# Optimization experiments

Measured on AMD Instinct MI355X. Metric: run time of the kernel, lower is better.

## Reference

```python
import jax, jax.numpy as jnp
import numpy as np

NMIX = 10  # mixtures in discretized mix of logistics


def _causal_mask(kh, kw, include_center):
    # rows strictly above center fully visible; center row left of center; optionally center
    m = np.zeros((kh, kw), dtype=np.float32)
    m[: kh // 2, :] = 1.0
    m[kh // 2, : kw // 2] = 1.0
    if include_center:
        m[kh // 2, kw // 2] = 1.0
    return jnp.asarray(m)[None, None]  # [1,1,kh,kw] broadcast over O,I


def _conv(x, w):
    return jax.lax.conv_general_dilated(
        x, w, (1, 1), 'SAME', dimension_numbers=('NCHW', 'OIHW', 'NCHW'))


def pixelcnn_params(x, w_in, w_blk, w_out1, w_out2):
    mA = _causal_mask(7, 7, False)
    mB = _causal_mask(3, 3, True)
    h = _conv(x, w_in * mA)                      # [B,160,H,W]
    for i in range(w_blk.shape[0]):              # 5 gated resnet blocks
        g = _conv(jax.nn.relu(h), w_blk[i] * mB)  # [B,320,H,W]
        a, b = jnp.split(g, 2, axis=1)
        h = h + jnp.tanh(a) * jax.nn.sigmoid(b)
    h = jax.nn.relu(_conv(jax.nn.relu(h), w_out1))
    return _conv(h, w_out2)                      # [B,100,H,W]


def dmol_log_prob(x, params):
    # x: [B,3,H,W] in [-1,1]; params: [B,100,H,W]; returns per-example log prob [B]
    B, C, H, W = x.shape
    l = jnp.transpose(params, (0, 2, 3, 1))       # [B,H,W,100]
    xt = jnp.transpose(x, (0, 2, 3, 1))           # [B,H,W,3]
    logit_probs = l[..., :NMIX]                   # [B,H,W,10]
    rest = l[..., NMIX:].reshape(B, H, W, 3, 3 * NMIX)
    means = rest[..., :NMIX]
    log_scales = jnp.maximum(rest[..., NMIX:2 * NMIX], -7.0)
    coeffs = jnp.tanh(rest[..., 2 * NMIX:])
    xe = xt[..., None]                            # [B,H,W,3,1]
    m1 = means[..., 0, :]
    m2 = means[..., 1, :] + coeffs[..., 0, :] * xe[..., 0, :]
    m3 = means[..., 2, :] + coeffs[..., 1, :] * xe[..., 0, :] + coeffs[..., 2, :] * xe[..., 1, :]
    means_adj = jnp.stack([m1, m2, m3], axis=3)   # [B,H,W,3,10]
    centered = xe - means_adj
    inv_stdv = jnp.exp(-log_scales)
    plus_in = inv_stdv * (centered + 1.0 / 255.0)
    min_in = inv_stdv * (centered - 1.0 / 255.0)
    cdf_delta = jax.nn.sigmoid(plus_in) - jax.nn.sigmoid(min_in)
    log_cdf_plus = plus_in - jax.nn.softplus(plus_in)
    log_one_minus_cdf_min = -jax.nn.softplus(min_in)
    mid_in = inv_stdv * centered
    log_pdf_mid = mid_in - log_scales - 2.0 * jax.nn.softplus(mid_in)
    log_prob_in = jnp.where(cdf_delta > 1e-5,
                            jnp.log(jnp.clip(cdf_delta, 1e-12, None)),
                            log_pdf_mid - np.float32(np.log(127.5)))
    log_probs_c = jnp.where(xe < -0.999, log_cdf_plus,
                            jnp.where(xe > 0.999, log_one_minus_cdf_min, log_prob_in))
    log_probs = jnp.sum(log_probs_c, axis=3) + jax.nn.log_softmax(logit_probs, axis=-1)
    lp = jax.scipy.special.logsumexp(log_probs, axis=-1)  # [B,H,W]
    return jnp.sum(lp, axis=(1, 2))                       # [B]


def setup_inputs() -> dict:
    key = jax.random.key(0)
    ks = jax.random.split(key, 5)
    F = 160
    return {
        'samples': jax.random.uniform(ks[0], (16, 3, 64, 64), dtype=jnp.float32),
        'w_in': jax.random.normal(ks[1], (F, 3, 7, 7), dtype=jnp.float32) * 0.05,
        'w_blk': jax.random.normal(ks[2], (5, 2 * F, F, 3, 3), dtype=jnp.float32) * 0.03,
        'w_out1': jax.random.normal(ks[3], (F, F, 1, 1), dtype=jnp.float32) * 0.05,
        'w_out2': jax.random.normal(ks[4], (100, F, 1, 1), dtype=jnp.float32) * 0.05,
    }


def reference(samples, w_in, w_blk, w_out1, w_out2):
    x = samples * 2.0 - 1.0
    params = pixelcnn_params(x, w_in, w_blk, w_out1, w_out2)
    return dmol_log_prob(x, params)
```

## Files before the change

kernel.cpp:

```cpp
#include <hip/hip_runtime.h>
#include <math.h>


using short8  = __attribute__((ext_vector_type(8))) short;
using short4v = __attribute__((ext_vector_type(4))) short;
using f32x4   = __attribute__((ext_vector_type(4))) float;
using f32x16  = __attribute__((ext_vector_type(16))) float;

static constexpr float L2E = 1.44269504088896f;
static constexpr float LN2 = 0.69314718055995f;

static constexpr int CPAD = 168;
static constexpr int RST  = 66 * CPAD;
static constexpr int IST  = 65 * RST;

__device__ __forceinline__ float fexp2(float x) { return __builtin_amdgcn_exp2f(x); }
__device__ __forceinline__ float flog2(float x) { return __builtin_amdgcn_logf(x); }
__device__ __forceinline__ float frcp(float x)  { return __builtin_amdgcn_rcpf(x); }
__device__ __forceinline__ float fexp(float x)  { return fexp2(x * L2E); }
__device__ __forceinline__ float flog(float x)  { return flog2(x) * LN2; }
__device__ __forceinline__ float fsigmoid(float x) { return frcp(1.f + fexp2(-x * L2E)); }
__device__ __forceinline__ float ftanh(float x)    { return 1.f - 2.f * frcp(1.f + fexp2(x * (2.f * L2E))); }
__device__ __forceinline__ float fsoftplus(float z) {
    float e = fexp2(-fabsf(z) * L2E);
    return fmaxf(z, 0.f) + flog2(1.f + e) * LN2;
}

__device__ __forceinline__ unsigned pk_bf16(float a, float b) {
    union { float f; unsigned u; } ua, ub; ua.f = a; ub.f = b;
    return __builtin_amdgcn_perm(ub.u + 0x7fffu, ua.u + 0x7fffu, 0x07060302u);
}

__device__ __forceinline__ short f2bf(float f) {
    union { float f; unsigned u; } v; v.f = f;
    unsigned r = (v.u + 0x7fffu + ((v.u >> 16) & 1u)) >> 16;
    return (short)r;
}

__device__ __forceinline__ float bf2f(unsigned short s) {
    union { unsigned u; float f; } v; v.u = ((unsigned)s) << 16; return v.f;
}

static constexpr size_t X_OFF    = 0;
static constexpr size_t WINP_OFF = 786432;
static constexpr size_t W1P_OFF  = 817152;
static constexpr size_t W2P_OFF  = 868352;
static constexpr size_t WPB_OFF  = 919552;
static constexpr size_t HA_OFF   = 3479552;
static constexpr size_t HB_OFF   = 24451072;
static constexpr size_t HRA_OFF  = 45422592;
static constexpr size_t HRB_OFF  = 68485632;

__global__ void k_prep(const float* __restrict__ s, float* __restrict__ x, int n) {
    int i = blockIdx.x * 256 + threadIdx.x;
    if (i < n) x[i] = 2.f * s[i] - 1.f;
}

__global__ void k_twb(const float* __restrict__ w, short* __restrict__ wP) {
    int idx = blockIdx.x * 256 + threadIdx.x;
    if (idx >= 5 * 100 * 320 * 8) return;
    int j  = idx & 7;
    int r  = idx >> 3;
    int oc = r % 320;
    int r2 = r / 320;
    int sp = r2 % 100;
    int i  = r2 / 100;
    int s = sp >> 1, pair = sp & 1;
    int k = s * 16 + pair * 8 + j;
    int tap = k / 160, ic = k - tap * 160;
    const int ky[5] = {0,0,0,1,1}, kx[5] = {0,1,2,0,1};
    float v = w[(((size_t)(i * 320 + oc) * 160 + ic) * 3 + ky[tap]) * 3 + kx[tap]];
    wP[idx] = f2bf(v);
}

__global__ void k_twin(const float* __restrict__ w, short* __restrict__ wP) {
    int idx = blockIdx.x * 256 + threadIdx.x;
    if (idx >= 3 * 160 * 32) return;
    int icl = idx & 31;
    int oc  = (idx >> 5) % 160;
    int kc  = idx / 5120;
    int k = kc * 32 + icl;
    short v = 0;
    if (k < 72) {
        int tap = k / 3, ic = k % 3;
        int ky = (tap < 21) ? tap / 7 : 3;
        int kx = (tap < 21) ? tap % 7 : tap - 21;
        v = f2bf(w[((oc * 3 + ic) * 7 + ky) * 7 + kx]);
    }
    wP[idx] = v;
}

__global__ void k_tw1(const float* __restrict__ w, short* __restrict__ wP) {
    int idx = blockIdx.x * 256 + threadIdx.x;
    if (idx >= 5 * 160 * 32) return;
    int icl = idx & 31;
    int oc  = (idx >> 5) % 160;
    int kc  = idx / 5120;
    wP[idx] = f2bf(w[oc * 160 + kc * 32 + icl]);
}

__global__ void k_tw2(const float* __restrict__ w, short* __restrict__ wP) {
    int idx = blockIdx.x * 256 + threadIdx.x;
    if (idx >= 5 * 160 * 32) return;
    int icl = idx & 31;
    int oc  = (idx >> 5) % 160;
    int kc  = idx / 5120;
    wP[idx] = (oc < 100) ? f2bf(w[oc * 160 + kc * 32 + icl]) : (short)0;
}

__global__ void k_halo(unsigned short* __restrict__ hrA, unsigned short* __restrict__ hrB) {
    int i = blockIdx.x * 256 + threadIdx.x;
    if (i >= 16 * 194 * CPAD) return;
    int c = i % CPAD;
    int r = (i / CPAD) % 194;
    int b = i / (CPAD * 194);
    int yp, xp;
    if (r < 66) { yp = 0; xp = r; }
    else { int rr = r - 66; yp = 1 + (rr >> 1); xp = (rr & 1) ? 65 : 0; }
    unsigned short* p = blockIdx.y ? hrB : hrA;
    p[((size_t)b * 65 + yp) * RST + (size_t)xp * CPAD + c] = 0;
}

__global__ __launch_bounds__(320) void k_convin(const float* __restrict__ X,
                                                const short* __restrict__ WINP,
                                                unsigned short* __restrict__ hout,
                                                unsigned short* __restrict__ hrout) {
    __shared__ float xls[3 * 4 * 40];
    __shared__ short Bls[32 * 104];
    int y = blockIdx.x >> 1, half = blockIdx.x & 1, b = blockIdx.y;
    int xbase = half * 32;
    int t = threadIdx.x;
    for (int i = t; i < 456; i += 320) {
        int col = i % 38; int r = (i / 38) % 4; int ic = i / 152;
        int xg = xbase + col - 3, yg = y + r - 3;
        float v = 0.f;
        if (xg >= 0 && xg < 64 && yg >= 0)
            v = X[((size_t)(b * 3 + ic) * 64 + yg) * 64 + xg];
        xls[(ic * 4 + r) * 40 + col] = v;
    }
    __syncthreads();
    for (int i = t; i < 3072; i += 320) {
        int k = i % 96; int px = i / 96;
        short v = 0;
        if (k < 72) {
            int tap = k / 3, ic = k % 3;
            int ky = (tap < 21) ? tap / 7 : 3;
            int kx = (tap < 21) ? tap % 7 : tap - 21;
            v = f2bf(xls[(ic * 4 + ky) * 40 + px + kx]);
        }
        Bls[px * 104 + k] = v;
    }
    __syncthreads();
    int lane = t & 63, w = t >> 6;
    int lx = lane & 15, q = lane >> 4;
    f32x4 acc[2][2] = {};
    const short* wl = WINP + lx * 32 + q * 8;
    #pragma unroll
    for (int kc = 0; kc < 3; ++kc) {
        short8 aF[2], bF[2];
        aF[0] = *(const short8*)(wl + (kc * 160 + 32 * w) * 32);
        aF[1] = *(const short8*)(wl + (kc * 160 + 32 * w + 16) * 32);
        #pragma unroll
        for (int nt = 0; nt < 2; ++nt)
            bF[nt] = *(const short8*)&Bls[(nt * 16 + lx) * 104 + kc * 32 + q * 8];
        #pragma unroll
        for (int mt = 0; mt < 2; ++mt)
            #pragma unroll
            for (int nt = 0; nt < 2; ++nt)
                acc[mt][nt] = __builtin_amdgcn_mfma_f32_16x16x32_bf16(
                    aF[mt], bF[nt], acc[mt][nt], 0, 0, 0);
    }
    size_t rowbase = ((size_t)(b * 64 + y)) * 64 * 160;
    size_t rbase   = ((size_t)b * 65 + (y + 1)) * RST;
    #pragma unroll
    for (int mt = 0; mt < 2; ++mt) {
        int c0 = 32 * w + mt * 16 + q * 4;
        #pragma unroll
        for (int nt = 0; nt < 2; ++nt) {
            int px = xbase + nt * 16 + lx;
            float o0 = acc[mt][nt][0], o1 = acc[mt][nt][1];
            float o2 = acc[mt][nt][2], o3 = acc[mt][nt][3];
            uint2 oh;
            oh.x = pk_bf16(o0, o1); oh.y = pk_bf16(o2, o3);
            *(uint2*)&hout[rowbase + (size_t)px * 160 + c0] = oh;
            uint2 orr;
            orr.x = pk_bf16(fmaxf(o0, 0.f), fmaxf(o1, 0.f));
            orr.y = pk_bf16(fmaxf(o2, 0.f), fmaxf(o3, 0.f));
            *(uint2*)&hrout[rbase + (size_t)(px + 1) * CPAD + c0] = orr;
        }
    }
}

__global__ __launch_bounds__(320, 4) void k_blk(const unsigned short* __restrict__ h_in,
                                                unsigned short* __restrict__ h_out,
                                                const unsigned short* __restrict__ hr_in,
                                                unsigned short* __restrict__ hr_out,
                                                const short* __restrict__ wP) {
    __shared__ short in_s[2 * RST];
    int y = blockIdx.x, b = blockIdx.y;
    int t = threadIdx.x;
    int lane = t & 63, w = t >> 6;
    {
        const unsigned short* src = hr_in + ((size_t)b * 65 + y) * RST;
        #pragma unroll
        for (int r = 0; r < 9; ++r) {
            int cb = __builtin_amdgcn_readfirstlane(r * 320 + w * 64);
            if (cb + lane < 2772) {
                __builtin_amdgcn_global_load_lds(
                    (const __attribute__((address_space(1))) unsigned int*)(src + (size_t)(cb + lane) * 8),
                    (__attribute__((address_space(3))) unsigned int*)(in_s + cb * 8),
                    16, 0, 0);
            }
        }
    }
    __syncthreads();

    int lm = lane & 31, pair = lane >> 5;
    f32x16 acc[2][2] = {};
    const short* waP = wP + pair * 2560 + (32 * w + lm) * 8;
    const int dxs[5] = {-1, 0, 1, -1, 0};
    const int rws[5] = {0, 0, 0, 1, 1};
    #pragma unroll
    for (int tap = 0; tap < 5; ++tap) {
        int rb0 = (rws[tap] * 66 + 1 + dxs[tap] + lm) * CPAD + pair * 8;
        #pragma unroll
        for (int si = 0; si < 10; ++si) {
            int s = tap * 10 + si;
            short8 aA = *(const short8*)(waP + (size_t)s * 5120);
            short8 aG = *(const short8*)(waP + 1280 + (size_t)s * 5120);
            short8 b0 = *(const short8*)&in_s[rb0 + si * 16];
            short8 b1 = *(const short8*)&in_s[rb0 + 32 * CPAD + si * 16];
            acc[0][0] = __builtin_amdgcn_mfma_f32_32x32x16_bf16(aA, b0, acc[0][0], 0, 0, 0);
            acc[0][1] = __builtin_amdgcn_mfma_f32_32x32x16_bf16(aA, b1, acc[0][1], 0, 0, 0);
            acc[1][0] = __builtin_amdgcn_mfma_f32_32x32x16_bf16(aG, b0, acc[1][0], 0, 0, 0);
            acc[1][1] = __builtin_amdgcn_mfma_f32_32x32x16_bf16(aG, b1, acc[1][1], 0, 0, 0);
        }
    }
    size_t rowbase = ((size_t)(b * 64 + y)) * 64 * 160;
    size_t rbase   = ((size_t)b * 65 + (y + 1)) * RST;
    #pragma unroll
    for (int n = 0; n < 2; ++n) {
        int px = n * 32 + lm;
        #pragma unroll
        for (int qd = 0; qd < 4; ++qd) {
            int c0 = 32 * w + qd * 8 + 4 * pair;
            size_t offh = rowbase + (size_t)px * 160 + c0;
            ushort4 hv = *(const ushort4*)&h_in[offh];
            float o0 = bf2f(hv.x) + ftanh(acc[0][n][qd * 4 + 0]) * fsigmoid(acc[1][n][qd * 4 + 0]);
            float o1 = bf2f(hv.y) + ftanh(acc[0][n][qd * 4 + 1]) * fsigmoid(acc[1][n][qd * 4 + 1]);
            float o2 = bf2f(hv.z) + ftanh(acc[0][n][qd * 4 + 2]) * fsigmoid(acc[1][n][qd * 4 + 2]);
            float o3 = bf2f(hv.w) + ftanh(acc[0][n][qd * 4 + 3]) * fsigmoid(acc[1][n][qd * 4 + 3]);
            uint2 oh;
            oh.x = pk_bf16(o0, o1); oh.y = pk_bf16(o2, o3);
            *(uint2*)&h_out[offh] = oh;
            uint2 orr;
            orr.x = pk_bf16(fmaxf(o0, 0.f), fmaxf(o1, 0.f));
            orr.y = pk_bf16(fmaxf(o2, 0.f), fmaxf(o3, 0.f));
            *(uint2*)&hr_out[rbase + (size_t)(px + 1) * CPAD + c0] = orr;
        }
    }
}

__global__ __launch_bounds__(320) void k_head(const unsigned short* __restrict__ hr,
                                              const short* __restrict__ W1P,
                                              const short* __restrict__ W2P,
                                              const float* __restrict__ X,
                                              float* __restrict__ out) {
    __shared__ char arena[14848];
    __shared__ short h2ls[32 * 168];
    short* hls = (short*)arena;
    float* Pls = (float*)arena;
    float* lpls = (float*)(arena + 13312);
    int y = blockIdx.x >> 1, half = blockIdx.x & 1, b = blockIdx.y;
    int xbase = half * 32;
    int t = threadIdx.x;
    size_t rbase = ((size_t)b * 65 + (y + 1)) * RST;
    for (int i = t; i < 640; i += 320) {
        int c8 = i % 20; int px = i / 20;
        uint4 v = *(const uint4*)&hr[rbase + (size_t)(xbase + px + 1) * CPAD + c8 * 8];
        *(uint4*)&hls[px * 168 + c8 * 8] = v;
    }
    __syncthreads();
    int lane = t & 63, w = t >> 6;
    int lx = lane & 15, q = lane >> 4;
    {
        f32x4 acc[2][2] = {};
        const short* wl = W1P + lx * 32 + q * 8;
        #pragma unroll
        for (int kc = 0; kc < 5; ++kc) {
            short8 aF[2], bF[2];
            aF[0] = *(const short8*)(wl + (kc * 160 + 32 * w) * 32);
            aF[1] = *(const short8*)(wl + (kc * 160 + 32 * w + 16) * 32);
            #pragma unroll
            for (int nt = 0; nt < 2; ++nt)
                bF[nt] = *(const short8*)&hls[(nt * 16 + lx) * 168 + kc * 32 + q * 8];
            #pragma unroll
            for (int mt = 0; mt < 2; ++mt)
                #pragma unroll
                for (int nt = 0; nt < 2; ++nt)
                    acc[mt][nt] = __builtin_amdgcn_mfma_f32_16x16x32_bf16(
                        aF[mt], bF[nt], acc[mt][nt], 0, 0, 0);
        }
        __syncthreads();
        #pragma unroll
        for (int mt = 0; mt < 2; ++mt) {
            int c0 = 32 * w + mt * 16 + q * 4;
            #pragma unroll
            for (int nt = 0; nt < 2; ++nt) {
                int px = nt * 16 + lx;
                union { short4v s; unsigned u[2]; } sv;
                sv.u[0] = pk_bf16(fmaxf(acc[mt][nt][0], 0.f), fmaxf(acc[mt][nt][1], 0.f));
                sv.u[1] = pk_bf16(fmaxf(acc[mt][nt][2], 0.f), fmaxf(acc[mt][nt][3], 0.f));
                *(short4v*)&h2ls[px * 168 + c0] = sv.s;
            }
        }
    }
    __syncthreads();
    {
        f32x4 acc[2][2] = {};
        const short* wl = W2P + lx * 32 + q * 8;
        #pragma unroll
        for (int kc = 0; kc < 5; ++kc) {
            short8 aF[2], bF[2];
            aF[0] = *(const short8*)(wl + (kc * 160 + 32 * w) * 32);
            aF[1] = *(const short8*)(wl + (kc * 160 + 32 * w + 16) * 32);
            #pragma unroll
            for (int nt = 0; nt < 2; ++nt)
                bF[nt] = *(const short8*)&h2ls[(nt * 16 + lx) * 168 + kc * 32 + q * 8];
            #pragma unroll
            for (int mt = 0; mt < 2; ++mt)
                #pragma unroll
                for (int nt = 0; nt < 2; ++nt)
                    acc[mt][nt] = __builtin_amdgcn_mfma_f32_16x16x32_bf16(
                        aF[mt], bF[nt], acc[mt][nt], 0, 0, 0);
        }
        #pragma unroll
        for (int mt = 0; mt < 2; ++mt) {
            int c0 = 32 * w + mt * 16 + q * 4;
            if (c0 < 100) {
                #pragma unroll
                for (int nt = 0; nt < 2; ++nt) {
                    int px = nt * 16 + lx;
                    float4 o;
                    o.x = acc[mt][nt][0]; o.y = acc[mt][nt][1];
                    o.z = acc[mt][nt][2]; o.w = acc[mt][nt][3];
                    *(float4*)&Pls[px * 104 + c0] = o;
                }
            }
        }
    }
    __syncthreads();
    const float LOG127P5 = 4.8481163504f;
    {
        int px = t & 31, m = t >> 5;
        const float* pp = &Pls[px * 104];
        float xs[3];
        #pragma unroll
        for (int c = 0; c < 3; ++c)
            xs[c] = X[((size_t)(b * 3 + c)) * 4096 + (size_t)y * 64 + xbase + px];
        float mx = pp[0];
        #pragma unroll
        for (int j = 1; j < 10; ++j) mx = fmaxf(mx, pp[j]);
        float se = 0.f;
        #pragma unroll
        for (int j = 0; j < 10; ++j) se += fexp(pp[j] - mx);
        float lse = mx + flog(se);
        float sum = pp[m] - lse;
        float mean0 = pp[10 + m];
        float mean1 = pp[40 + m];
        float mean2 = pp[70 + m];
        float ls0 = fmaxf(pp[20 + m], -7.f);
        float ls1 = fmaxf(pp[50 + m], -7.f);
        float ls2 = fmaxf(pp[80 + m], -7.f);
        float c0 = ftanh(pp[30 + m]);
        float c1 = ftanh(pp[60 + m]);
        float c2 = ftanh(pp[90 + m]);
        float mu[3], lsv[3];
        mu[0] = mean0;
        mu[1] = mean1 + c0 * xs[0];
        mu[2] = mean2 + c1 * xs[0] + c2 * xs[1];
        lsv[0] = ls0; lsv[1] = ls1; lsv[2] = ls2;
        #pragma unroll
        for (int ci = 0; ci < 3; ++ci) {
            float cent = xs[ci] - mu[ci];
            float inv = fexp(-lsv[ci]);
            float plus_in = inv * (cent + 1.f / 255.f);
            float min_in = inv * (cent - 1.f / 255.f);
            float cdf_delta = fsigmoid(plus_in) - fsigmoid(min_in);
            float log_cdf_plus = plus_in - fsoftplus(plus_in);
            float log_om_cdf = -fsoftplus(min_in);
            float mid = inv * cent;
            float log_pdf_mid = mid - lsv[ci] - 2.f * fsoftplus(mid);
            float lpi = (cdf_delta > 1e-5f) ? flog(fmaxf(cdf_delta, 1e-12f))
                                            : (log_pdf_mid - LOG127P5);
            float lpc = (xs[ci] < -0.999f) ? log_cdf_plus
                       : ((xs[ci] > 0.999f) ? log_om_cdf : lpi);
            sum += lpc;
        }
        lpls[px * 12 + m] = sum;
    }
    __syncthreads();
    if (t < 32) {
        int px = t;
        float mx2 = lpls[px * 12];
        #pragma unroll
        for (int m = 1; m < 10; ++m) mx2 = fmaxf(mx2, lpls[px * 12 + m]);
        float se2 = 0.f;
        #pragma unroll
        for (int m = 0; m < 10; ++m) se2 += fexp(lpls[px * 12 + m] - mx2);
        float lp = mx2 + flog(se2);
        lp += __shfl_down(lp, 16, 32);
        lp += __shfl_down(lp, 8, 32);
        lp += __shfl_down(lp, 4, 32);
        lp += __shfl_down(lp, 2, 32);
        lp += __shfl_down(lp, 1, 32);
        if (t == 0) atomicAdd(&out[b], lp);
    }
}

extern "C" void kernel_launch(void* const* d_in, const int* in_sizes, int n_in,
                              void* d_out, int out_size, void* d_ws, size_t ws_size,
                              hipStream_t stream) {
    const float* samples = (const float*)d_in[0];
    const float* w_in    = (const float*)d_in[1];
    const float* w_blk   = (const float*)d_in[2];
    const float* w_out1  = (const float*)d_in[3];
    const float* w_out2  = (const float*)d_in[4];
    char* ws = (char*)d_ws;
    float* X    = (float*)(ws + X_OFF);
    short* WINP = (short*)(ws + WINP_OFF);
    short* W1P  = (short*)(ws + W1P_OFF);
    short* W2P  = (short*)(ws + W2P_OFF);
    short* WPB  = (short*)(ws + WPB_OFF);
    unsigned short* HA  = (unsigned short*)(ws + HA_OFF);
    unsigned short* HB  = (unsigned short*)(ws + HB_OFF);
    unsigned short* HRA = (unsigned short*)(ws + HRA_OFF);
    unsigned short* HRB = (unsigned short*)(ws + HRB_OFF);
    float* fout = (float*)d_out;

    k_prep<<<768, 256, 0, stream>>>(samples, X, 16 * 3 * 4096);
    k_twb<<<5000, 256, 0, stream>>>(w_blk, WPB);
    k_twin<<<60, 256, 0, stream>>>(w_in, WINP);
    k_tw1<<<100, 256, 0, stream>>>(w_out1, W1P);
    k_tw2<<<100, 256, 0, stream>>>(w_out2, W2P);
    k_halo<<<dim3((16 * 194 * CPAD + 255) / 256, 2), 256, 0, stream>>>(HRA, HRB);

    k_convin<<<dim3(128, 16), 320, 0, stream>>>(X, WINP, HA, HRA);

    unsigned short* a = HA;  unsigned short* bq = HB;
    unsigned short* ra = HRA; unsigned short* rb = HRB;
    for (int i = 0; i < 5; i++) {
        k_blk<<<dim3(64, 16), 320, 0, stream>>>(a, bq, ra, rb, WPB + (size_t)i * 256000);
        unsigned short* tmp = a; a = bq; bq = tmp;
        unsigned short* tr = ra; ra = rb; rb = tr;
    }
    hipMemsetAsync(d_out, 0, (size_t)out_size * sizeof(float), stream);
    k_head<<<dim3(128, 16), 320, 0, stream>>>(ra, W1P, W2P, X, fout);
}
```

Baseline: 461.1 us.

## Fold input scaling into consumers and prefetch weights and residual in gated block kernel

Removes the separate k_prep kernel and its workspace buffer, computing 2*s-1 inline inside the first conv and the head kernels. In k_blk, the residual h_in values are loaded before the LDS barrier so their latency overlaps the async LDS fill. Weight fragments are software-prefetched one step ahead, and the starting tap is staggered per wave to spread LDS bank and cache traffic. Launch bounds drop from 4 to 3 blocks per CU to give the extra live registers room, at the cost of lower occupancy.

```diff
diff --git a/kernel.cpp b/kernel.cpp
--- a/kernel.cpp
+++ b/kernel.cpp
@@ -41,20 +41,14 @@
     union { unsigned u; float f; } v; v.u = ((unsigned)s) << 16; return v.f;
 }
 
-static constexpr size_t X_OFF    = 0;
-static constexpr size_t WINP_OFF = 786432;
-static constexpr size_t W1P_OFF  = 817152;
-static constexpr size_t W2P_OFF  = 868352;
-static constexpr size_t WPB_OFF  = 919552;
-static constexpr size_t HA_OFF   = 3479552;
-static constexpr size_t HB_OFF   = 24451072;
-static constexpr size_t HRA_OFF  = 45422592;
-static constexpr size_t HRB_OFF  = 68485632;
-
-__global__ void k_prep(const float* __restrict__ s, float* __restrict__ x, int n) {
-    int i = blockIdx.x * 256 + threadIdx.x;
-    if (i < n) x[i] = 2.f * s[i] - 1.f;
-}
+static constexpr size_t WINP_OFF = 0;
+static constexpr size_t W1P_OFF  = 30720;
+static constexpr size_t W2P_OFF  = 81920;
+static constexpr size_t WPB_OFF  = 133120;
+static constexpr size_t HA_OFF   = 2693120;
+static constexpr size_t HB_OFF   = 23664640;
+static constexpr size_t HRA_OFF  = 44636160;
+static constexpr size_t HRB_OFF  = 67699200;
 
 __global__ void k_twb(const float* __restrict__ w, short* __restrict__ wP) {
     int idx = blockIdx.x * 256 + threadIdx.x;
@@ -121,7 +115,7 @@
     p[((size_t)b * 65 + yp) * RST + (size_t)xp * CPAD + c] = 0;
 }
 
-__global__ __launch_bounds__(320) void k_convin(const float* __restrict__ X,
+__global__ __launch_bounds__(320) void k_convin(const float* __restrict__ S,
                                                 const short* __restrict__ WINP,
                                                 unsigned short* __restrict__ hout,
                                                 unsigned short* __restrict__ hrout) {
@@ -135,7 +129,7 @@
         int xg = xbase + col - 3, yg = y + r - 3;
         float v = 0.f;
         if (xg >= 0 && xg < 64 && yg >= 0)
-            v = X[((size_t)(b * 3 + ic) * 64 + yg) * 64 + xg];
+            v = 2.f * S[((size_t)(b * 3 + ic) * 64 + yg) * 64 + xg] - 1.f;
         xls[(ic * 4 + r) * 40 + col] = v;
     }
     __syncthreads();
@@ -191,7 +185,7 @@
     }
 }
 
-__global__ __launch_bounds__(320, 4) void k_blk(const unsigned short* __restrict__ h_in,
+__global__ __launch_bounds__(320, 3) void k_blk(const unsigned short* __restrict__ h_in,
                                                 unsigned short* __restrict__ h_out,
                                                 const unsigned short* __restrict__ hr_in,
                                                 unsigned short* __restrict__ hr_out,
@@ -213,21 +207,38 @@
             }
         }
     }
-    __syncthreads();
-
     int lm = lane & 31, pair = lane >> 5;
+    size_t rowbase = ((size_t)(b * 64 + y)) * 64 * 160;
+    ushort4 hv[2][4];
+    #pragma unroll
+    for (int n = 0; n < 2; ++n) {
+        int px = n * 32 + lm;
+        #pragma unroll
+        for (int qd = 0; qd < 4; ++qd) {
+            int c0 = 32 * w + qd * 8 + 4 * pair;
+            hv[n][qd] = *(const ushort4*)&h_in[rowbase + (size_t)px * 160 + c0];
+        }
+    }
+    __syncthreads();
+
     f32x16 acc[2][2] = {};
     const short* waP = wP + pair * 2560 + (32 * w + lm) * 8;
     const int dxs[5] = {-1, 0, 1, -1, 0};
     const int rws[5] = {0, 0, 0, 1, 1};
     #pragma unroll
-    for (int tap = 0; tap < 5; ++tap) {
+    for (int tt = 0; tt < 5; ++tt) {
+        int tap = tt + w;  tap = (tap >= 5) ? tap - 5 : tap;
         int rb0 = (rws[tap] * 66 + 1 + dxs[tap] + lm) * CPAD + pair * 8;
+        int s0 = tap * 10;
+        short8 pA = *(const short8*)(waP + (size_t)s0 * 5120);
+        short8 pG = *(const short8*)(waP + 1280 + (size_t)s0 * 5120);
         #pragma unroll
         for (int si = 0; si < 10; ++si) {
-            int s = tap * 10 + si;
-            short8 aA = *(const short8*)(waP + (size_t)s * 5120);
-            short8 aG = *(const short8*)(waP + 1280 + (size_t)s * 5120);
+            short8 aA = pA, aG = pG;
+            if (si < 9) {
+                pA = *(const short8*)(waP + (size_t)(s0 + si + 1) * 5120);
+                pG = *(const short8*)(waP + 1280 + (size_t)(s0 + si + 1) * 5120);
+            }
             short8 b0 = *(const short8*)&in_s[rb0 + si * 16];
             short8 b1 = *(const short8*)&in_s[rb0 + 32 * CPAD + si * 16];
             acc[0][0] = __builtin_amdgcn_mfma_f32_32x32x16_bf16(aA, b0, acc[0][0], 0, 0, 0);
@@ -236,8 +247,7 @@
             acc[1][1] = __builtin_amdgcn_mfma_f32_32x32x16_bf16(aG, b1, acc[1][1], 0, 0, 0);
         }
     }
-    size_t rowbase = ((size_t)(b * 64 + y)) * 64 * 160;
-    size_t rbase   = ((size_t)b * 65 + (y + 1)) * RST;
+    size_t rbase = ((size_t)b * 65 + (y + 1)) * RST;
     #pragma unroll
     for (int n = 0; n < 2; ++n) {
         int px = n * 32 + lm;
@@ -245,11 +255,10 @@
         for (int qd = 0; qd < 4; ++qd) {
             int c0 = 32 * w + qd * 8 + 4 * pair;
             size_t offh = rowbase + (size_t)px * 160 + c0;
-            ushort4 hv = *(const ushort4*)&h_in[offh];
-            float o0 = bf2f(hv.x) + ftanh(acc[0][n][qd * 4 + 0]) * fsigmoid(acc[1][n][qd * 4 + 0]);
-            float o1 = bf2f(hv.y) + ftanh(acc[0][n][qd * 4 + 1]) * fsigmoid(acc[1][n][qd * 4 + 1]);
-            float o2 = bf2f(hv.z) + ftanh(acc[0][n][qd * 4 + 2]) * fsigmoid(acc[1][n][qd * 4 + 2]);
-            float o3 = bf2f(hv.w) + ftanh(acc[0][n][qd * 4 + 3]) * fsigmoid(acc[1][n][qd * 4 + 3]);
+            float o0 = bf2f(hv[n][qd].x) + ftanh(acc[0][n][qd * 4 + 0]) * fsigmoid(acc[1][n][qd * 4 + 0]);
+            float o1 = bf2f(hv[n][qd].y) + ftanh(acc[0][n][qd * 4 + 1]) * fsigmoid(acc[1][n][qd * 4 + 1]);
+            float o2 = bf2f(hv[n][qd].z) + ftanh(acc[0][n][qd * 4 + 2]) * fsigmoid(acc[1][n][qd * 4 + 2]);
+            float o3 = bf2f(hv[n][qd].w) + ftanh(acc[0][n][qd * 4 + 3]) * fsigmoid(acc[1][n][qd * 4 + 3]);
             uint2 oh;
             oh.x = pk_bf16(o0, o1); oh.y = pk_bf16(o2, o3);
             *(uint2*)&h_out[offh] = oh;
@@ -264,7 +273,7 @@
 __global__ __launch_bounds__(320) void k_head(const unsigned short* __restrict__ hr,
                                               const short* __restrict__ W1P,
                                               const short* __restrict__ W2P,
-                                              const float* __restrict__ X,
+                                              const float* __restrict__ S,
                                               float* __restrict__ out) {
     __shared__ char arena[14848];
     __shared__ short h2ls[32 * 168];
@@ -357,7 +366,7 @@
         float xs[3];
         #pragma unroll
         for (int c = 0; c < 3; ++c)
-            xs[c] = X[((size_t)(b * 3 + c)) * 4096 + (size_t)y * 64 + xbase + px];
+            xs[c] = 2.f * S[((size_t)(b * 3 + c)) * 4096 + (size_t)y * 64 + xbase + px] - 1.f;
         float mx = pp[0];
         #pragma unroll
         for (int j = 1; j < 10; ++j) mx = fmaxf(mx, pp[j]);
@@ -427,7 +436,6 @@
     const float* w_out1  = (const float*)d_in[3];
     const float* w_out2  = (const float*)d_in[4];
     char* ws = (char*)d_ws;
-    float* X    = (float*)(ws + X_OFF);
     short* WINP = (short*)(ws + WINP_OFF);
     short* W1P  = (short*)(ws + W1P_OFF);
     short* W2P  = (short*)(ws + W2P_OFF);
@@ -438,14 +446,13 @@
     unsigned short* HRB = (unsigned short*)(ws + HRB_OFF);
     float* fout = (float*)d_out;
 
-    k_prep<<<768, 256, 0, stream>>>(samples, X, 16 * 3 * 4096);
     k_twb<<<5000, 256, 0, stream>>>(w_blk, WPB);
     k_twin<<<60, 256, 0, stream>>>(w_in, WINP);
     k_tw1<<<100, 256, 0, stream>>>(w_out1, W1P);
     k_tw2<<<100, 256, 0, stream>>>(w_out2, W2P);
     k_halo<<<dim3((16 * 194 * CPAD + 255) / 256, 2), 256, 0, stream>>>(HRA, HRB);
 
-    k_convin<<<dim3(128, 16), 320, 0, stream>>>(X, WINP, HA, HRA);
+    k_convin<<<dim3(128, 16), 320, 0, stream>>>(samples, WINP, HA, HRA);
 
     unsigned short* a = HA;  unsigned short* bq = HB;
     unsigned short* ra = HRA; unsigned short* rb = HRB;
@@ -455,5 +462,5 @@
         unsigned short* tr = ra; ra = rb; rb = tr;
     }
     hipMemsetAsync(d_out, 0, (size_t)out_size * sizeof(float), stream);
-    k_head<<<dim3(128, 16), 320, 0, stream>>>(ra, W1P, W2P, X, fout);
-}
+    k_head<<<dim3(128, 16), 320, 0, stream>>>(ra, W1P, W2P, samples, fout);
+}
```

Result: no change. 459.2 us (-0.4%).
